# Kernel optimization log

Hardware: AMD Instinct MI355X
Metric: run time of the kernel (lower is better)

Reference implementation:

```python
import jax, jax.numpy as jnp
import numpy as np

B, S, DIM = 2, 2048, 2048
N_HEADS, N_KV_HEADS = 16, 8
HEAD_DIM = DIM // N_HEADS          # 128
KV_DIM = N_KV_HEADS * HEAD_DIM     # 1024
SKETCH = 64
ROPE_THETA = 500000.0
INV_SQRT_HD = np.float32(1.0 / np.sqrt(HEAD_DIM))


def sketch_mm(A, Sm, Bm):
    """projection_sketch_mm: approximate A @ Bm as (A S / k) @ (S^T B).
    A: (b, n, d), Sm: (b, d, k), Bm: (d, m)."""
    AS = jnp.matmul(A, Sm) / Sm.shape[-1]      # (b, n, k)
    SB = jnp.einsum('bdk,dm->bkm', Sm, Bm)     # (b, k, m)
    return jnp.matmul(AS, SB)                  # (b, n, m)


def apply_rotary(x, freqs_cis):
    """Faithful port of the module's apply_rotary_emb for one tensor.
    x: (b, s, h, hd); freqs_cis: (s, hd//2, 2) with [...,0]=cos, [...,1]=sin."""
    x2 = x.reshape(*x.shape[:-1], HEAD_DIM // 2, 2)
    f = freqs_cis[None, :, None, :, :]         # broadcast over batch & heads
    c, s = f[..., 0], f[..., 1]
    x0, x1 = x2[..., 0], x2[..., 1]
    row1 = x0 * c + x1 * s                     # dot(x, [cos, sin])
    row0 = x0 * s - x1 * c                     # dot(x, [sin, -cos]) (flip + negate)
    return jnp.stack([row0, row1], axis=-1).reshape(x.shape)


def setup_inputs() -> dict:
    key = jax.random.key(0)
    ks = jax.random.split(key, 9)
    x = jax.random.normal(ks[0], (B, S, DIM), jnp.float32)
    wq = jax.random.normal(ks[1], (DIM, DIM), jnp.float32) / np.float32(np.sqrt(DIM))
    wk = jax.random.normal(ks[2], (KV_DIM, DIM), jnp.float32) / np.float32(np.sqrt(DIM))
    wv = jax.random.normal(ks[3], (KV_DIM, DIM), jnp.float32) / np.float32(np.sqrt(DIM))
    wo = jax.random.normal(ks[4], (DIM, DIM), jnp.float32) / np.float32(np.sqrt(DIM))
    # gaussian sketch matrices (sketch_mode='gaussian'), one per batch element
    Sq = jax.random.normal(ks[5], (B, DIM, SKETCH), jnp.float32)
    Sk = jax.random.normal(ks[6], (B, DIM, SKETCH), jnp.float32)
    Sv = jax.random.normal(ks[7], (B, DIM, SKETCH), jnp.float32)
    So = jax.random.normal(ks[8], (B, DIM, SKETCH), jnp.float32)
    # RoPE table: (S, HEAD_DIM//2, 2) = stack([cos, sin])
    pos = jnp.arange(S, dtype=jnp.float32)
    inv = 1.0 / (ROPE_THETA ** (jnp.arange(0, HEAD_DIM, 2, dtype=jnp.float32) / HEAD_DIM))
    ang = pos[:, None] * inv[None, :]
    freqs_cis = jnp.stack([jnp.cos(ang), jnp.sin(ang)], axis=-1)
    return {"x": x, "wq": wq, "wk": wk, "wv": wv, "wo": wo,
            "Sq": Sq, "Sk": Sk, "Sv": Sv, "So": So, "freqs_cis": freqs_cis}


def reference(x, wq, wk, wv, wo, Sq, Sk, Sv, So, freqs_cis):
    b, s, _ = x.shape
    # RLALinear projections via projection sketch (weight stored (out, in) -> use W.T)
    xq = sketch_mm(x, Sq, wq.T).reshape(b, s, N_HEADS, HEAD_DIM)
    xk = sketch_mm(x, Sk, wk.T).reshape(b, s, N_KV_HEADS, HEAD_DIM)
    xv = sketch_mm(x, Sv, wv.T).reshape(b, s, N_KV_HEADS, HEAD_DIM)
    xq = apply_rotary(xq, freqs_cis)
    xk = apply_rotary(xk, freqs_cis)
    # repeat_kv: each kv head repeated n_rep times consecutively
    n_rep = N_HEADS // N_KV_HEADS
    k = jnp.repeat(xk, n_rep, axis=2)
    v = jnp.repeat(xv, n_rep, axis=2)
    q = xq.transpose(0, 2, 1, 3)               # (b, h, s, d)
    k = k.transpose(0, 2, 1, 3)
    v = v.transpose(0, 2, 1, 3)
    scores = jnp.einsum('bhqd,bhkd->bhqk', q, k) * INV_SQRT_HD
    mask = jnp.tril(jnp.ones((s, s), dtype=bool))
    scores = jnp.where(mask[None, None], scores, jnp.finfo(scores.dtype).min)
    probs = jax.nn.softmax(scores, axis=-1)
    out = jnp.einsum('bhqk,bhkd->bhqd', probs, v)
    out = out.transpose(0, 2, 1, 3).reshape(b, s, DIM)
    # output RLALinear via sketch
    return sketch_mm(out, So, wo.T)
```

## Files before the change

### kernel.cpp

```cpp
#include <hip/hip_runtime.h>
#include <math.h>

#define S_LEN 2048
#define DIM   2048
#define NH    16
#define NKV   8
#define HD    128
#define SKETCH 64
#define KV_DIM 1024
#define SCALE (0.08838834764831845f * 1.4426950408889634f)

typedef _Float16 half8_t  __attribute__((ext_vector_type(8)));
typedef __bf16   bf8_t    __attribute__((ext_vector_type(8)));
typedef __bf16   bf4_t    __attribute__((ext_vector_type(4)));
typedef float    f32x16_t __attribute__((ext_vector_type(16)));
typedef unsigned int uint4_t __attribute__((ext_vector_type(4)));

__global__ __launch_bounds__(256) void sbas_mfma(
    const float* __restrict__ x,
    const float* __restrict__ Sq, const float* __restrict__ Sk,
    const float* __restrict__ Sv, const float* __restrict__ So,
    const float* __restrict__ wq, const float* __restrict__ wk,
    const float* __restrict__ wv, const float* __restrict__ wo,
    float* __restrict__ SBq, float* __restrict__ SBk,
// ... 218 lines not shown
    }
    __syncthreads();
#pragma unroll
    for (int ks = 0; ks < 4; ++ks) {
      bf8_t ah = *(const bf8_t*)&Xh[w * 32 + l31][ks * 16 + h32 * 8];
      bf8_t al = *(const bf8_t*)&Xl[w * 32 + l31][ks * 16 + h32 * 8];
#pragma unroll
      for (int nt = 0; nt < 2; ++nt) {
        bf8_t bh_ = *(const bf8_t*)&Sth[nt * 32 + l31][ks * 16 + h32 * 8];
        bf8_t bl_ = *(const bf8_t*)&Stl[nt * 32 + l31][ks * 16 + h32 * 8];
        acc[nt] = __builtin_amdgcn_mfma_f32_32x32x16_bf16(ah, bh_, acc[nt], 0, 0, 0);
        acc[nt] = __builtin_amdgcn_mfma_f32_32x32x16_bf16(al, bh_, acc[nt], 0, 0, 0);
        acc[nt] = __builtin_amdgcn_mfma_f32_32x32x16_bf16(ah, bl_, acc[nt], 0, 0, 0);
      }
    }
    __syncthreads();
  }
#pragma unroll
  for (int nt = 0; nt < 2; ++nt)
#pragma unroll
    for (int r = 0; r < 16; ++r) {
      int row = row0 + w * 32 + (r & 3) + 8 * (r >> 2) + 4 * h32;
      atomicAdd(&OUT[(size_t)row * SKETCH + nt * 32 + l31],
                acc[nt][r] * (1.0f / 64.0f));
    }
}

__device__ __forceinline__ void proj_gemm_core(
    const float* __restrict__ ASb, const float* __restrict__ SBb, int Mout,
    int s0, int n0, __bf16* ASh, __bf16* ASl, __bf16* SBth, __bf16* SBtl,
    f32x16_t acc[2]) {
  const int tid = threadIdx.x, ln = tid & 63, w = tid >> 6;
  const int l31 = ln & 31, h32 = ln >> 5;
#pragma unroll
  for (int it = 0; it < 8; ++it) {
    int i = tid + it * 256;
    int r = i >> 4, c4 = (i & 15) << 2;
    float4 v = *(const float4*)(ASb + (size_t)(s0 + r) * SKETCH + c4);
    bf4_t hx, lx;
    float vv[4] = {v.x, v.y, v.z, v.w};
#pragma unroll
    for (int j = 0; j < 4; ++j) {
      __bf16 hh = (__bf16)vv[j];
      hx[j] = hh; lx[j] = (__bf16)(vv[j] - (float)hh);
    }
    *(bf4_t*)&ASh[r * 72 + c4] = hx;
    *(bf4_t*)&ASl[r * 72 + c4] = lx;
  }
#pragma unroll
  for (int it = 0; it < 4; ++it) {
    int i = tid + it * 256;
    int k = i >> 4, c4 = (i & 15) << 2;
    float4 v = *(const float4*)(SBb + (size_t)k * Mout + n0 + c4);
    float vv[4] = {v.x, v.y, v.z, v.w};
#pragma unroll
    for (int j = 0; j < 4; ++j) {
      __bf16 hh = (__bf16)vv[j];
      SBth[(c4 + j) * 72 + k] = hh;
      SBtl[(c4 + j) * 72 + k] = (__bf16)(vv[j] - (float)hh);
    }
  }
  __syncthreads();
#pragma unroll
  for (int ks = 0; ks < 4; ++ks) {
    bf8_t ah = *(const bf8_t*)&ASh[(w * 32 + l31) * 72 + ks * 16 + h32 * 8];
    bf8_t al = *(const bf8_t*)&ASl[(w * 32 + l31) * 72 + ks * 16 + h32 * 8];
#pragma unroll
    for (int nt = 0; nt < 2; ++nt) {
      bf8_t bh_ = *(const bf8_t*)&SBth[(nt * 32 + l31) * 72 + ks * 16 + h32 * 8];
      bf8_t bl_ = *(const bf8_t*)&SBtl[(nt * 32 + l31) * 72 + ks * 16 + h32 * 8];
      acc[nt] = __builtin_amdgcn_mfma_f32_32x32x16_bf16(ah, bh_, acc[nt], 0, 0, 0);
      acc[nt] = __builtin_amdgcn_mfma_f32_32x32x16_bf16(al, bh_, acc[nt], 0, 0, 0);
      acc[nt] = __builtin_amdgcn_mfma_f32_32x32x16_bf16(ah, bl_, acc[nt], 0, 0, 0);
    }
  }
}

__global__ __launch_bounds__(256) void proj_qkv(
    const float* __restrict__ ASq, const float* __restrict__ ASk,
    const float* __restrict__ ASv,
    const float* __restrict__ SBq, const float* __restrict__ SBk,
    const float* __restrict__ SBv,
    const float* __restrict__ freqs,
    _Float16* __restrict__ Qf, _Float16* __restrict__ Kf,
    _Float16* __restrict__ Vf) {
  __shared__ __bf16 ASh[128 * 72], ASl[128 * 72], SBth[64 * 72], SBtl[64 * 72];
  const int b = blockIdx.z, y = blockIdx.y;
  const float *AS, *SB;
  int Mout, nh, mt;
  _Float16* OUT;
  bool rope;
  if (y < 32)      { AS = ASq; SB = SBq; Mout = DIM;    nh = NH;  mt = y;      OUT = Qf; rope = true; }
  else if (y < 48) { AS = ASk; SB = SBk; Mout = KV_DIM; nh = NKV; mt = y - 32; OUT = Kf; rope = true; }
  else             { AS = ASv; SB = SBv; Mout = KV_DIM; nh = NKV; mt = y - 48; OUT = Vf; rope = false; }
  const int s0 = blockIdx.x * 128, n0 = mt * 64;
  f32x16_t acc[2];
#pragma unroll
  for (int nt = 0; nt < 2; ++nt)
#pragma unroll
    for (int r = 0; r < 16; ++r) acc[nt][r] = 0.0f;
  proj_gemm_core(AS + (size_t)b * S_LEN * SKETCH, SB + (size_t)b * SKETCH * Mout,
                 Mout, s0, n0, ASh, ASl, SBth, SBtl, acc);
  const int tid = threadIdx.x, ln = tid & 63, w = tid >> 6;
  const int l31 = ln & 31, h32 = ln >> 5;
  const bool meven = (l31 & 1) == 0;
#pragma unroll
  for (int nt = 0; nt < 2; ++nt) {
    const int m = n0 + nt * 32 + l31;
    const int h = m >> 7, hd = m & (HD - 1);
    const int p = hd >> 1;
#pragma unroll
    for (int r = 0; r < 16; ++r) {
      const int s = s0 + w * 32 + (r & 3) + 8 * (r >> 2) + 4 * h32;
      float v = acc[nt][r];
      float outv;
      if (rope) {
        int pi = __builtin_bit_cast(int, v);
        float part = __builtin_bit_cast(float, __builtin_amdgcn_ds_swizzle(pi, 0x041F));
        float co = freqs[((size_t)s * 64 + p) * 2 + 0];
        float si = freqs[((size_t)s * 64 + p) * 2 + 1];
        outv = meven ? (v * si - part * co) : (part * co + v * si);
      } else {
        outv = v;
      }
      OUT[(((size_t)b * nh + h) * S_LEN + s) * HD + hd] = (_Float16)outv;
    }
  }
}

__global__ __launch_bounds__(256) void proj_out(
    const float* __restrict__ ASo, const float* __restrict__ SBo,
    float* __restrict__ out) {
  __shared__ __bf16 ASh[128 * 72], ASl[128 * 72], SBth[64 * 72], SBtl[64 * 72];
  const int b = blockIdx.z;
  const int s0 = blockIdx.x * 128, n0 = blockIdx.y * 64;
  f32x16_t acc[2];
#pragma unroll
  for (int nt = 0; nt < 2; ++nt)
#pragma unroll
    for (int r = 0; r < 16; ++r) acc[nt][r] = 0.0f;
  proj_gemm_core(ASo + (size_t)b * S_LEN * SKETCH, SBo + (size_t)b * SKETCH * DIM,
                 DIM, s0, n0, ASh, ASl, SBth, SBtl, acc);
  const int tid = threadIdx.x, ln = tid & 63, w = tid >> 6;
  const int l31 = ln & 31, h32 = ln >> 5;
#pragma unroll
  for (int nt = 0; nt < 2; ++nt)
#pragma unroll
    for (int r = 0; r < 16; ++r) {
      const int s = s0 + w * 32 + (r & 3) + 8 * (r >> 2) + 4 * h32;
      out[((size_t)b * S_LEN + s) * DIM + n0 + nt * 32 + l31] = acc[nt][r];
    }
}

#define KTT 64

__global__ __launch_bounds__(256, 2) void attn_mfma(
    const _Float16* __restrict__ Qf, const _Float16* __restrict__ Kf,
    const _Float16* __restrict__ Vf, float* __restrict__ O) {
  const int bh = blockIdx.x;
  const int b = bh >> 4, h = bh & 15, g = h >> 1;
  const int qt = 31 - (int)blockIdx.y;
  const int q0 = qt * 64;

  const int tid = threadIdx.x;
  const int ln = tid & 63, w = tid >> 6;
  const int wg = w & 1, half = w >> 1;
  const int l31 = ln & 31, h32 = ln >> 5;
  const bool hb = (h32 != 0);

  __shared__ __align__(16) char smem[65536];
  char* KsH = smem + half * 16384;
  char* VtH = smem + 32768 + half * 16384;
  float* Pl = (float*)smem;
  float* Ot = (float*)smem;

  const _Float16* Kp = Kf + (size_t)(b * NKV + g) * S_LEN * HD;
  const _Float16* Vp = Vf + (size_t)(b * NKV + g) * S_LEN * HD;

  half8_t qfr[8];
  {
    const size_t qrow = (size_t)(b * NH + h) * S_LEN + q0 + wg * 32 + l31;
#pragma unroll
    for (int ks = 0; ks < 8; ++ks)
      qfr[ks] = *(const half8_t*)(Qf + qrow * HD + ks * 16 + h32 * 8);
  }

  float mrow = -1.0e30f, lrow = 0.0f;
  f32x16_t o[4];
#pragma unroll
  for (int dt = 0; dt < 4; ++dt)
#pragma unroll
    for (int r = 0; r < 16; ++r) o[dt][r] = 0.0f;

  const int wq_start = q0 + wg * 32;
  const int qq = wq_start + l31;
  const int nkt = qt + 1;
  const int nk0 = (nkt + 1) >> 1, nk1 = nkt >> 1;

  half8_t kregA[4], vregA[4], kregB[4], vregB[4];

#define LOADK(dst, t)                                                          \
  _Pragma("unroll") for (int it_ = 0; it_ < 4; ++it_) {                        \
    int i_ = tid + it_ * 256;                                                  \
    dst[it_] = *(const half8_t*)(Kp + (size_t)((t) * 64 + (i_ >> 4)) * HD +    \
                                 ((i_ & 15) << 3));                            \
  }
#define LOADV(dst, t)                                                          \
  _Pragma("unroll") for (int it_ = 0; it_ < 4; ++it_) {                        \
    int i_ = tid + it_ * 256;                                                  \
    dst[it_] = *(const half8_t*)(Vp + (size_t)((t) * 64 + (i_ & 63)) * HD +    \
                                 ((i_ >> 6) << 3));                            \
  }
#define STOREK(base, src)                                                      \
  _Pragma("unroll") for (int it_ = 0; it_ < 4; ++it_) {                        \
    int i_ = tid + it_ * 256;                                                  \
    int row_ = i_ >> 4, gg_ = (i_ & 15) ^ (row_ & 15);                         \
    *(half8_t*)((base) + row_ * 256 + (gg_ << 4)) = src[it_];                  \
  }
#define STOREV(base, src)                                                      \
  _Pragma("unroll") for (int it_ = 0; it_ < 4; ++it_) {                        \
    int i_ = tid + it_ * 256;                                                  \
    int k_ = i_ & 63, d0_ = (i_ >> 6) << 3;                                    \
    _Pragma("unroll") for (int j_ = 0; j_ < 8; ++j_) {                         \
      int d_ = d0_ + j_, gg_ = (k_ >> 3) ^ (d_ & 7);                           \
      *(_Float16*)((base) + d_ * 128 + (gg_ << 4) + ((k_ & 7) << 1)) =         \
          src[it_][j_];                                                        \
    }                                                                          \
  }

  LOADK(kregA, 0); LOADV(vregA, 0);
  if (nk1 > 0) { LOADK(kregB, nk0); LOADV(vregB, nk0); }
  STOREK(smem, kregA); STOREV(smem + 32768, vregA);
  if (nk1 > 0) { STOREK(smem + 16384, kregB); STOREV(smem + 49152, vregB); }
  __syncthreads();

  for (int i = 0; i < nk0; ++i) {
    const bool pfA = (i + 1 < nk0), pfB = (i + 1 < nk1);
    if (pfA) { LOADK(kregA, i + 1); LOADV(vregA, i + 1); }
    if (pfB) { LOADK(kregB, nk0 + i + 1); LOADV(vregB, nk0 + i + 1); }

    const int myt = half ? (nk0 + i) : i;
    const int k0 = myt * KTT;
    const bool active = (half ? (i < nk1) : true) && (k0 < wq_start + 32);

    if (active) {
      f32x16_t sc[2];
#pragma unroll
      for (int nt = 0; nt < 2; ++nt)
#pragma unroll
        for (int r = 0; r < 16; ++r) sc[nt][r] = 0.0f;
#pragma unroll
      for (int ks = 0; ks < 8; ++ks)
#pragma unroll
        for (int nt = 0; nt < 2; ++nt) {
          const int kk = nt * 32 + l31;
          half8_t kf = *(const half8_t*)(
              KsH + kk * 256 + ((((ks << 1) + h32) ^ (kk & 15)) << 4));
          sc[nt] = __builtin_amdgcn_mfma_f32_32x32x16_f16(kf, qfr[ks], sc[nt], 0, 0, 0);
        }
      const bool needMask = (k0 + KTT > wq_start);
#pragma unroll
      for (int nt = 0; nt < 2; ++nt)
#pragma unroll
        for (int r = 0; r < 16; ++r) {
          int kg = k0 + nt * 32 + (r & 3) + 8 * (r >> 2) + 4 * h32;
          float s = sc[nt][r] * SCALE;
          sc[nt][r] = (!needMask || kg <= qq) ? s : -1.0e30f;
        }
      float ml = sc[0][0];
#pragma unroll
      for (int r = 1; r < 16; ++r) ml = fmaxf(ml, sc[0][r]);
#pragma unroll
      for (int r = 0; r < 16; ++r) ml = fmaxf(ml, sc[1][r]);
      ml = fmaxf(ml, __shfl_xor(ml, 32));
      float mn = fmaxf(mrow, ml);
      float alpha = __builtin_amdgcn_exp2f(mrow - mn);
      mrow = mn;
      float ps = 0.0f;
#pragma unroll
      for (int nt = 0; nt < 2; ++nt)
#pragma unroll
        for (int r = 0; r < 16; ++r) {
          float p = __builtin_amdgcn_exp2f(sc[nt][r] - mn);
          sc[nt][r] = p;
          ps += p;
        }
      ps += __shfl_xor(ps, 32);
      lrow = lrow * alpha + ps;
#pragma unroll
      for (int dt = 0; dt < 4; ++dt)
#pragma unroll
        for (int r = 0; r < 16; ++r) o[dt][r] *= alpha;

      unsigned int pk[2][8];
#pragma unroll
      for (int nt = 0; nt < 2; ++nt)
#pragma unroll
        for (int gq = 0; gq < 8; ++gq)
          pk[nt][gq] = __builtin_bit_cast(
              unsigned int,
              __builtin_amdgcn_cvt_pkrtz(sc[nt][2 * gq], sc[nt][2 * gq + 1]));
#pragma unroll
      for (int ks2 = 0; ks2 < 4; ++ks2) {
        const int nt = ks2 >> 1, a = ks2 & 1;
        unsigned int own0 = hb ? pk[nt][4 * a + 2] : pk[nt][4 * a + 0];
        unsigned int own1 = hb ? pk[nt][4 * a + 3] : pk[nt][4 * a + 1];
        unsigned int oth0 = hb ? pk[nt][4 * a + 0] : pk[nt][4 * a + 2];
        unsigned int oth1 = hb ? pk[nt][4 * a + 1] : pk[nt][4 * a + 3];
        unsigned int rcv0 = __shfl_xor(oth0, 32);
        unsigned int rcv1 = __shfl_xor(oth1, 32);
        uint4_t fu;
        fu.x = hb ? rcv0 : own0;
        fu.y = hb ? rcv1 : own1;
        fu.z = hb ? own0 : rcv0;
        fu.w = hb ? own1 : rcv1;
        half8_t pf = __builtin_bit_cast(half8_t, fu);
#pragma unroll
        for (int dt = 0; dt < 4; ++dt) {
          const int d = dt * 32 + l31;
          half8_t vf = *(const half8_t*)(
              VtH + d * 128 + ((((ks2 << 1) + h32) ^ (d & 7)) << 4));
          o[dt] = __builtin_amdgcn_mfma_f32_32x32x16_f16(vf, pf, o[dt], 0, 0, 0);
        }
      }
    }

    if (pfA || pfB) {
      __syncthreads();
      if (pfA) { STOREK(smem, kregA); STOREV(smem + 32768, vregA); }
      if (pfB) { STOREK(smem + 16384, kregB); STOREV(smem + 49152, vregB); }
      __syncthreads();
    }
  }

  __syncthreads();
  if (w >= 2) {
    float* dst = Pl + ((size_t)(w - 2) * 64 + ln) * 68;
#pragma unroll
    for (int dt = 0; dt < 4; ++dt)
#pragma unroll
      for (int gq = 0; gq < 4; ++gq) {
        float4 vv;
        vv.x = o[dt][4 * gq + 0]; vv.y = o[dt][4 * gq + 1];
        vv.z = o[dt][4 * gq + 2]; vv.w = o[dt][4 * gq + 3];
        *(float4*)&dst[dt * 16 + gq * 4] = vv;
      }
    dst[64] = mrow; dst[65] = lrow;
  }
  __syncthreads();
  if (w < 2) {
    const float* src = Pl + ((size_t)w * 64 + ln) * 68;
    float m2 = src[64], l2 = src[65];
    float mn = fmaxf(mrow, m2);
    float a1 = __builtin_amdgcn_exp2f(mrow - mn);
    float a2 = __builtin_amdgcn_exp2f(m2 - mn);
    lrow = lrow * a1 + l2 * a2;
#pragma unroll
    for (int dt = 0; dt < 4; ++dt)
#pragma unroll
      for (int r = 0; r < 16; ++r)
        o[dt][r] = o[dt][r] * a1 + src[dt * 16 + r] * a2;
  }

  const float linv = 1.0f / lrow;
  const int s_l = tid >> 5, d_l = tid & 31;
#pragma unroll
  for (int dt = 0; dt < 4; ++dt) {
    __syncthreads();
    if (w < 2) {
#pragma unroll
      for (int gq = 0; gq < 4; ++gq) {
        float4 vv;
        vv.x = o[dt][4 * gq + 0] * linv;
        vv.y = o[dt][4 * gq + 1] * linv;
        vv.z = o[dt][4 * gq + 2] * linv;
        vv.w = o[dt][4 * gq + 3] * linv;
        *(float4*)&Ot[(wg * 32 + l31) * 36 + 8 * gq + 4 * h32] = vv;
      }
    }
    __syncthreads();
#pragma unroll
    for (int i = 0; i < 8; ++i) {
      int s = s_l + 8 * i;
      float v = Ot[s * 36 + d_l];
      O[((size_t)b * S_LEN + q0 + s) * DIM + h * HD + dt * 32 + d_l] = v;
    }
  }
#undef LOADK
#undef LOADV
#undef STOREK
#undef STOREV
}

extern "C" void kernel_launch(void* const* d_in, const int* in_sizes, int n_in,
                              void* d_out, int out_size, void* d_ws, size_t ws_size,
                              hipStream_t stream) {
  const float* x     = (const float*)d_in[0];
  const float* wq    = (const float*)d_in[1];
  const float* wk    = (const float*)d_in[2];
  const float* wv    = (const float*)d_in[3];
  const float* wo    = (const float*)d_in[4];
  const float* Sq    = (const float*)d_in[5];
  const float* Sk    = (const float*)d_in[6];
  const float* Sv    = (const float*)d_in[7];
  const float* So    = (const float*)d_in[8];
  const float* freqs = (const float*)d_in[9];
  float* out = (float*)d_out;

  const size_t AS_E = (size_t)2 * S_LEN * SKETCH;
  const size_t SBQ_E = (size_t)2 * SKETCH * DIM;
  const size_t SBK_E = (size_t)2 * SKETCH * KV_DIM;

  float* fp = (float*)d_ws;
  float* ASq = fp;  fp += AS_E;
  float* ASk = fp;  fp += AS_E;
  float* ASv = fp;  fp += AS_E;
  float* ASo = fp;  fp += AS_E;
  float* SBq = fp;  fp += SBQ_E;
  float* SBk = fp;  fp += SBK_E;
  float* SBv = fp;  fp += SBK_E;
  float* SBo = fp;  fp += SBQ_E;
  float* ATT = fp;  fp += (size_t)2 * S_LEN * DIM;
  _Float16* hp = (_Float16*)fp;
  _Float16* Qfb = hp; hp += (size_t)2 * NH  * S_LEN * HD;
  _Float16* Kfb = hp; hp += (size_t)2 * NKV * S_LEN * HD;
  _Float16* Vfb = hp; hp += (size_t)2 * NKV * S_LEN * HD;

  (void)hipMemsetAsync(ASq, 0, (4 * AS_E + 2 * SBQ_E + 2 * SBK_E) * sizeof(float), stream);

  hipLaunchKernelGGL(sbas_mfma, dim3(640), dim3(256), 0, stream,
                     x, Sq, Sk, Sv, So, wq, wk, wv, wo,
                     SBq, SBk, SBv, SBo, ASq, ASk, ASv);
  hipLaunchKernelGGL(proj_qkv, dim3(16, 64, 2), dim3(256), 0, stream,
                     ASq, ASk, ASv, SBq, SBk, SBv, freqs, Qfb, Kfb, Vfb);
  hipLaunchKernelGGL(attn_mfma, dim3(32, 32), dim3(256), 0, stream,
                     Qfb, Kfb, Vfb, ATT);
  hipLaunchKernelGGL(as_mfma, dim3(32, 8), dim3(256), 0, stream, ATT, So, ASo);
  hipLaunchKernelGGL(proj_out, dim3(16, 32, 2), dim3(256), 0, stream, ASo, SBo, out);
}
```

Before: 396.6 us.

## Shrink attention key tile to 32 with padded LDS and lazy rescaling

Cuts the attention key/value tile from 64 to 32 rows, lowering shared memory from 64KB to 35KB and raising the launch-bounds occupancy hint from 2 to 3 blocks. It also replaces the XOR-swizzled LDS layouts with padded row strides. The online softmax now rescales the output accumulator only when the running max grows by more than a threshold. The cost is twice as many loop iterations and barriers per tile, plus possible bank conflicts from the padding layout. The split of keys between the two half-blocks changes from an even split to a fixed offset of nk tiles.

```diff
diff --git a/kernel.cpp b/kernel.cpp
--- a/kernel.cpp
+++ b/kernel.cpp
@@ -394,9 +394,9 @@
     }
 }
 
-#define KTT 64
-
-__global__ __launch_bounds__(256, 2) void attn_mfma(
+#define KTT 32
+
+__global__ __launch_bounds__(256, 3) void attn_mfma(
     const _Float16* __restrict__ Qf, const _Float16* __restrict__ Kf,
     const _Float16* __restrict__ Vf, float* __restrict__ O) {
   const int bh = blockIdx.x;
@@ -410,9 +410,9 @@
   const int l31 = ln & 31, h32 = ln >> 5;
   const bool hb = (h32 != 0);
 
-  __shared__ __align__(16) char smem[65536];
-  char* KsH = smem + half * 16384;
-  char* VtH = smem + 32768 + half * 16384;
+  __shared__ __align__(16) char smem[35840];
+  char* KsH = smem + half * 8704;
+  char* VtH = smem + 17408 + half * 9216;
   float* Pl = (float*)smem;
   float* Ot = (float*)smem;
 
@@ -436,119 +436,106 @@
 
   const int wq_start = q0 + wg * 32;
   const int qq = wq_start + l31;
-  const int nkt = qt + 1;
-  const int nk0 = (nkt + 1) >> 1, nk1 = nkt >> 1;
-
-  half8_t kregA[4], vregA[4], kregB[4], vregB[4];
+  const int nk = qt + 1;
+
+  half8_t kregA[2], vregA[2], kregB[2], vregB[2];
 
 #define LOADK(dst, t)                                                          \
-  _Pragma("unroll") for (int it_ = 0; it_ < 4; ++it_) {                        \
+  _Pragma("unroll") for (int it_ = 0; it_ < 2; ++it_) {                        \
     int i_ = tid + it_ * 256;                                                  \
-    dst[it_] = *(const half8_t*)(Kp + (size_t)((t) * 64 + (i_ >> 4)) * HD +    \
+    dst[it_] = *(const half8_t*)(Kp + (size_t)((t) * 32 + (i_ >> 4)) * HD +    \
                                  ((i_ & 15) << 3));                            \
   }
 #define LOADV(dst, t)                                                          \
-  _Pragma("unroll") for (int it_ = 0; it_ < 4; ++it_) {                        \
+  _Pragma("unroll") for (int it_ = 0; it_ < 2; ++it_) {                        \
     int i_ = tid + it_ * 256;                                                  \
-    dst[it_] = *(const half8_t*)(Vp + (size_t)((t) * 64 + (i_ & 63)) * HD +    \
-                                 ((i_ >> 6) << 3));                            \
+    dst[it_] = *(const half8_t*)(Vp + (size_t)((t) * 32 + (i_ & 31)) * HD +    \
+                                 ((i_ >> 5) << 3));                            \
   }
 #define STOREK(base, src)                                                      \
-  _Pragma("unroll") for (int it_ = 0; it_ < 4; ++it_) {                        \
+  _Pragma("unroll") for (int it_ = 0; it_ < 2; ++it_) {                        \
     int i_ = tid + it_ * 256;                                                  \
-    int row_ = i_ >> 4, gg_ = (i_ & 15) ^ (row_ & 15);                         \
-    *(half8_t*)((base) + row_ * 256 + (gg_ << 4)) = src[it_];                  \
+    int row_ = i_ >> 4, gr_ = i_ & 15;                                         \
+    *(half8_t*)((base) + row_ * 272 + (gr_ << 4)) = src[it_];                  \
   }
 #define STOREV(base, src)                                                      \
-  _Pragma("unroll") for (int it_ = 0; it_ < 4; ++it_) {                        \
+  _Pragma("unroll") for (int it_ = 0; it_ < 2; ++it_) {                        \
     int i_ = tid + it_ * 256;                                                  \
-    int k_ = i_ & 63, d0_ = (i_ >> 6) << 3;                                    \
+    int k_ = i_ & 31, d0_ = (i_ >> 5) << 3;                                    \
     _Pragma("unroll") for (int j_ = 0; j_ < 8; ++j_) {                         \
-      int d_ = d0_ + j_, gg_ = (k_ >> 3) ^ (d_ & 7);                           \
-      *(_Float16*)((base) + d_ * 128 + (gg_ << 4) + ((k_ & 7) << 1)) =         \
-          src[it_][j_];                                                        \
+      *(_Float16*)((base) + (d0_ + j_) * 72 + (k_ << 1)) = src[it_][j_];       \
     }                                                                          \
   }
 
   LOADK(kregA, 0); LOADV(vregA, 0);
-  if (nk1 > 0) { LOADK(kregB, nk0); LOADV(vregB, nk0); }
-  STOREK(smem, kregA); STOREV(smem + 32768, vregA);
-  if (nk1 > 0) { STOREK(smem + 16384, kregB); STOREV(smem + 49152, vregB); }
+  LOADK(kregB, nk); LOADV(vregB, nk);
+  STOREK(smem, kregA); STOREV(smem + 17408, vregA);
+  STOREK(smem + 8704, kregB); STOREV(smem + 17408 + 9216, vregB);
   __syncthreads();
 
-  for (int i = 0; i < nk0; ++i) {
-    const bool pfA = (i + 1 < nk0), pfB = (i + 1 < nk1);
-    if (pfA) { LOADK(kregA, i + 1); LOADV(vregA, i + 1); }
-    if (pfB) { LOADK(kregB, nk0 + i + 1); LOADV(vregB, nk0 + i + 1); }
-
-    const int myt = half ? (nk0 + i) : i;
-    const int k0 = myt * KTT;
-    const bool active = (half ? (i < nk1) : true) && (k0 < wq_start + 32);
+  for (int i = 0; i < nk; ++i) {
+    const bool pf = (i + 1 < nk);
+    if (pf) {
+      LOADK(kregA, i + 1); LOADV(vregA, i + 1);
+      LOADK(kregB, nk + i + 1); LOADV(vregB, nk + i + 1);
+    }
+
+    const int t = half ? (nk + i) : i;
+    const int k0 = t * KTT;
+    const bool active = (k0 < wq_start + 32);
 
     if (active) {
-      f32x16_t sc[2];
-#pragma unroll
-      for (int nt = 0; nt < 2; ++nt)
-#pragma unroll
-        for (int r = 0; r < 16; ++r) sc[nt][r] = 0.0f;
-#pragma unroll
-      for (int ks = 0; ks < 8; ++ks)
-#pragma unroll
-        for (int nt = 0; nt < 2; ++nt) {
-          const int kk = nt * 32 + l31;
-          half8_t kf = *(const half8_t*)(
-              KsH + kk * 256 + ((((ks << 1) + h32) ^ (kk & 15)) << 4));
-          sc[nt] = __builtin_amdgcn_mfma_f32_32x32x16_f16(kf, qfr[ks], sc[nt], 0, 0, 0);
-        }
+      f32x16_t sc;
+#pragma unroll
+      for (int r = 0; r < 16; ++r) sc[r] = 0.0f;
+#pragma unroll
+      for (int ks = 0; ks < 8; ++ks) {
+        half8_t kf = *(const half8_t*)(KsH + l31 * 272 + ((ks * 16 + h32 * 8) << 1));
+        sc = __builtin_amdgcn_mfma_f32_32x32x16_f16(kf, qfr[ks], sc, 0, 0, 0);
+      }
       const bool needMask = (k0 + KTT > wq_start);
 #pragma unroll
-      for (int nt = 0; nt < 2; ++nt)
-#pragma unroll
-        for (int r = 0; r < 16; ++r) {
-          int kg = k0 + nt * 32 + (r & 3) + 8 * (r >> 2) + 4 * h32;
-          float s = sc[nt][r] * SCALE;
-          sc[nt][r] = (!needMask || kg <= qq) ? s : -1.0e30f;
-        }
-      float ml = sc[0][0];
-#pragma unroll
-      for (int r = 1; r < 16; ++r) ml = fmaxf(ml, sc[0][r]);
-#pragma unroll
-      for (int r = 0; r < 16; ++r) ml = fmaxf(ml, sc[1][r]);
+      for (int r = 0; r < 16; ++r) {
+        int kg = k0 + (r & 3) + 8 * (r >> 2) + 4 * h32;
+        float s = sc[r] * SCALE;
+        sc[r] = (!needMask || kg <= qq) ? s : -1.0e30f;
+      }
+      float ml = sc[0];
+#pragma unroll
+      for (int r = 1; r < 16; ++r) ml = fmaxf(ml, sc[r]);
       ml = fmaxf(ml, __shfl_xor(ml, 32));
-      float mn = fmaxf(mrow, ml);
-      float alpha = __builtin_amdgcn_exp2f(mrow - mn);
-      mrow = mn;
+      if (!__all(ml <= mrow + 8.0f)) {
+        float mn = fmaxf(mrow, ml);
+        float alpha = __builtin_amdgcn_exp2f(mrow - mn);
+        mrow = mn;
+        lrow *= alpha;
+#pragma unroll
+        for (int dt = 0; dt < 4; ++dt)
+#pragma unroll
+          for (int r = 0; r < 16; ++r) o[dt][r] *= alpha;
+      }
       float ps = 0.0f;
 #pragma unroll
-      for (int nt = 0; nt < 2; ++nt)
-#pragma unroll
-        for (int r = 0; r < 16; ++r) {
-          float p = __builtin_amdgcn_exp2f(sc[nt][r] - mn);
-          sc[nt][r] = p;
-          ps += p;
-        }
+      for (int r = 0; r < 16; ++r) {
+        float p = __builtin_amdgcn_exp2f(sc[r] - mrow);
+        sc[r] = p;
+        ps += p;
+      }
       ps += __shfl_xor(ps, 32);
-      lrow = lrow * alpha + ps;
-#pragma unroll
-      for (int dt = 0; dt < 4; ++dt)
-#pragma unroll
-        for (int r = 0; r < 16; ++r) o[dt][r] *= alpha;
-
-      unsigned int pk[2][8];
-#pragma unroll
-      for (int nt = 0; nt < 2; ++nt)
-#pragma unroll
-        for (int gq = 0; gq < 8; ++gq)
-          pk[nt][gq] = __builtin_bit_cast(
-              unsigned int,
-              __builtin_amdgcn_cvt_pkrtz(sc[nt][2 * gq], sc[nt][2 * gq + 1]));
-#pragma unroll
-      for (int ks2 = 0; ks2 < 4; ++ks2) {
-        const int nt = ks2 >> 1, a = ks2 & 1;
-        unsigned int own0 = hb ? pk[nt][4 * a + 2] : pk[nt][4 * a + 0];
-        unsigned int own1 = hb ? pk[nt][4 * a + 3] : pk[nt][4 * a + 1];
-        unsigned int oth0 = hb ? pk[nt][4 * a + 0] : pk[nt][4 * a + 2];
-        unsigned int oth1 = hb ? pk[nt][4 * a + 1] : pk[nt][4 * a + 3];
+      lrow += ps;
+
+      unsigned int pk[8];
+#pragma unroll
+      for (int gq = 0; gq < 8; ++gq)
+        pk[gq] = __builtin_bit_cast(
+            unsigned int,
+            __builtin_amdgcn_cvt_pkrtz(sc[2 * gq], sc[2 * gq + 1]));
+#pragma unroll
+      for (int ks2 = 0; ks2 < 2; ++ks2) {
+        unsigned int own0 = hb ? pk[4 * ks2 + 2] : pk[4 * ks2 + 0];
+        unsigned int own1 = hb ? pk[4 * ks2 + 3] : pk[4 * ks2 + 1];
+        unsigned int oth0 = hb ? pk[4 * ks2 + 0] : pk[4 * ks2 + 2];
+        unsigned int oth1 = hb ? pk[4 * ks2 + 1] : pk[4 * ks2 + 3];
         unsigned int rcv0 = __shfl_xor(oth0, 32);
         unsigned int rcv1 = __shfl_xor(oth1, 32);
         uint4_t fu;
@@ -556,21 +543,20 @@
         fu.y = hb ? rcv1 : own1;
         fu.z = hb ? own0 : rcv0;
         fu.w = hb ? own1 : rcv1;
-        half8_t pf = __builtin_bit_cast(half8_t, fu);
+        half8_t pf16 = __builtin_bit_cast(half8_t, fu);
 #pragma unroll
         for (int dt = 0; dt < 4; ++dt) {
-          const int d = dt * 32 + l31;
           half8_t vf = *(const half8_t*)(
-              VtH + d * 128 + ((((ks2 << 1) + h32) ^ (d & 7)) << 4));
-          o[dt] = __builtin_amdgcn_mfma_f32_32x32x16_f16(vf, pf, o[dt], 0, 0, 0);
-        }
-      }
-    }
-
-    if (pfA || pfB) {
+              VtH + (dt * 32 + l31) * 72 + ((ks2 * 16 + h32 * 8) << 1));
+          o[dt] = __builtin_amdgcn_mfma_f32_32x32x16_f16(vf, pf16, o[dt], 0, 0, 0);
+        }
+      }
+    }
+
+    if (pf) {
       __syncthreads();
-      if (pfA) { STOREK(smem, kregA); STOREV(smem + 32768, vregA); }
-      if (pfB) { STOREK(smem + 16384, kregB); STOREV(smem + 49152, vregB); }
+      STOREK(smem, kregA); STOREV(smem + 17408, vregA);
+      STOREK(smem + 8704, kregB); STOREV(smem + 17408 + 9216, vregB);
       __syncthreads();
     }
   }
```

After: 419.2 us. 1.06x slower.

## Load K fragments directly to registers, pad V smem, add lazy softmax rescale

Applied to the files above, without the earlier changes.

The attention kernel now loads K MFMA operand fragments straight from global memory into registers, ping-ponging between two register sets through a manually unrolled loop, so K no longer goes through shared memory. V is stored transposed in a padded layout (row stride 144 bytes) instead of an XOR swizzle, which shrinks LDS from 64KB to 36KB. The online softmax skips the rescale of the accumulators and row sum unless the new max exceeds the running max by more than 8 in log2 units. In exchange, register pressure rises (two sets of 16 half8 K fragments) and the K global loads are uncoalesced per lane. The lazy rescale lets unnormalized exponentials grow up to 2^8 before renormalizing, which risks precision loss in the fp16 probability conversion.

```diff
diff --git a/kernel.cpp b/kernel.cpp
--- a/kernel.cpp
+++ b/kernel.cpp
@@ -395,6 +395,89 @@
 }
 
 #define KTT 64
+#define VTP 144
+
+__device__ __forceinline__ void attn_step(
+    const half8_t (&kf)[2][8], const half8_t (&qfr)[8], const char* VtH,
+    int k0, int wq_start, int qq, bool hb, int h32, int l31,
+    float& mrow, float& lrow, f32x16_t (&o)[4]) {
+  f32x16_t sc[2];
+#pragma unroll
+  for (int nt = 0; nt < 2; ++nt)
+#pragma unroll
+    for (int r = 0; r < 16; ++r) sc[nt][r] = 0.0f;
+#pragma unroll
+  for (int ks = 0; ks < 8; ++ks)
+#pragma unroll
+    for (int nt = 0; nt < 2; ++nt)
+      sc[nt] = __builtin_amdgcn_mfma_f32_32x32x16_f16(kf[nt][ks], qfr[ks], sc[nt], 0, 0, 0);
+  const bool needMask = (k0 + KTT > wq_start);
+#pragma unroll
+  for (int nt = 0; nt < 2; ++nt)
+#pragma unroll
+    for (int r = 0; r < 16; ++r) {
+      int kg = k0 + nt * 32 + (r & 3) + 8 * (r >> 2) + 4 * h32;
+      float s = sc[nt][r] * SCALE;
+      sc[nt][r] = (!needMask || kg <= qq) ? s : -1.0e30f;
+    }
+  float ml = sc[0][0];
+#pragma unroll
+  for (int r = 1; r < 16; ++r) ml = fmaxf(ml, sc[0][r]);
+#pragma unroll
+  for (int r = 0; r < 16; ++r) ml = fmaxf(ml, sc[1][r]);
+  ml = fmaxf(ml, __shfl_xor(ml, 32));
+  if (!__all(ml <= mrow + 8.0f)) {
+    float mn = fmaxf(mrow, ml);
+    float alpha = __builtin_amdgcn_exp2f(mrow - mn);
+    mrow = mn;
+    lrow *= alpha;
+#pragma unroll
+    for (int dt = 0; dt < 4; ++dt)
+#pragma unroll
+      for (int r = 0; r < 16; ++r) o[dt][r] *= alpha;
+  }
+  float ps = 0.0f;
+#pragma unroll
+  for (int nt = 0; nt < 2; ++nt)
+#pragma unroll
+    for (int r = 0; r < 16; ++r) {
+      float p = __builtin_amdgcn_exp2f(sc[nt][r] - mrow);
+      sc[nt][r] = p;
+      ps += p;
+    }
+  ps += __shfl_xor(ps, 32);
+  lrow += ps;
+  unsigned int pk[2][8];
+#pragma unroll
+  for (int nt = 0; nt < 2; ++nt)
+#pragma unroll
+    for (int gq = 0; gq < 8; ++gq)
+      pk[nt][gq] = __builtin_bit_cast(
+          unsigned int,
+          __builtin_amdgcn_cvt_pkrtz(sc[nt][2 * gq], sc[nt][2 * gq + 1]));
+#pragma unroll
+  for (int ks2 = 0; ks2 < 4; ++ks2) {
+    const int nt = ks2 >> 1, a = ks2 & 1;
+    unsigned int own0 = hb ? pk[nt][4 * a + 2] : pk[nt][4 * a + 0];
+    unsigned int own1 = hb ? pk[nt][4 * a + 3] : pk[nt][4 * a + 1];
+    unsigned int oth0 = hb ? pk[nt][4 * a + 0] : pk[nt][4 * a + 2];
+    unsigned int oth1 = hb ? pk[nt][4 * a + 1] : pk[nt][4 * a + 3];
+    unsigned int rcv0 = __shfl_xor(oth0, 32);
+    unsigned int rcv1 = __shfl_xor(oth1, 32);
+    uint4_t fu;
+    fu.x = hb ? rcv0 : own0;
+    fu.y = hb ? rcv1 : own1;
+    fu.z = hb ? own0 : rcv0;
+    fu.w = hb ? own1 : rcv1;
+    half8_t pf16 = __builtin_bit_cast(half8_t, fu);
+#pragma unroll
+    for (int dt = 0; dt < 4; ++dt) {
+      half8_t vf = *(const half8_t*)(
+          VtH + (dt * 32 + l31) * VTP + ((ks2 * 16 + h32 * 8) << 1));
+      o[dt] = __builtin_amdgcn_mfma_f32_32x32x16_f16(vf, pf16, o[dt], 0, 0, 0);
+    }
+  }
+}
 
 __global__ __launch_bounds__(256, 2) void attn_mfma(
     const _Float16* __restrict__ Qf, const _Float16* __restrict__ Kf,
@@ -410,9 +493,8 @@
   const int l31 = ln & 31, h32 = ln >> 5;
   const bool hb = (h32 != 0);
 
-  __shared__ __align__(16) char smem[65536];
-  char* KsH = smem + half * 16384;
-  char* VtH = smem + 32768 + half * 16384;
+  __shared__ __align__(16) char smem[36864];
+  char* VtH = smem + half * 18432;
   float* Pl = (float*)smem;
   float* Ot = (float*)smem;
 
@@ -439,140 +521,79 @@
   const int nkt = qt + 1;
   const int nk0 = (nkt + 1) >> 1, nk1 = nkt >> 1;
 
-  half8_t kregA[4], vregA[4], kregB[4], vregB[4];
-
-#define LOADK(dst, t)                                                          \
+  half8_t ka[2][8], kb[2][8];
+  half8_t vsA[4], vsB[4];
+
+#define LOADKF(dst, ti)                                                        \
+  _Pragma("unroll") for (int nt_ = 0; nt_ < 2; ++nt_)                          \
+  _Pragma("unroll") for (int ks_ = 0; ks_ < 8; ++ks_)                          \
+    dst[nt_][ks_] = *(const half8_t*)(                                         \
+        Kp + (size_t)((ti) * 64 + nt_ * 32 + l31) * HD + ks_ * 16 + h32 * 8);
+#define LOADVS(dst, ti)                                                        \
   _Pragma("unroll") for (int it_ = 0; it_ < 4; ++it_) {                        \
     int i_ = tid + it_ * 256;                                                  \
-    dst[it_] = *(const half8_t*)(Kp + (size_t)((t) * 64 + (i_ >> 4)) * HD +    \
-                                 ((i_ & 15) << 3));                            \
-  }
-#define LOADV(dst, t)                                                          \
-  _Pragma("unroll") for (int it_ = 0; it_ < 4; ++it_) {                        \
-    int i_ = tid + it_ * 256;                                                  \
-    dst[it_] = *(const half8_t*)(Vp + (size_t)((t) * 64 + (i_ & 63)) * HD +    \
-                                 ((i_ >> 6) << 3));                            \
-  }
-#define STOREK(base, src)                                                      \
-  _Pragma("unroll") for (int it_ = 0; it_ < 4; ++it_) {                        \
-    int i_ = tid + it_ * 256;                                                  \
-    int row_ = i_ >> 4, gg_ = (i_ & 15) ^ (row_ & 15);                         \
-    *(half8_t*)((base) + row_ * 256 + (gg_ << 4)) = src[it_];                  \
-  }
-#define STOREV(base, src)                                                      \
+    dst[it_] = *(const half8_t*)(                                              \
+        Vp + (size_t)((ti) * 64 + (i_ & 63)) * HD + ((i_ >> 6) << 3));         \
+  }
+#define STOREVS(base, src)                                                     \
   _Pragma("unroll") for (int it_ = 0; it_ < 4; ++it_) {                        \
     int i_ = tid + it_ * 256;                                                  \
     int k_ = i_ & 63, d0_ = (i_ >> 6) << 3;                                    \
-    _Pragma("unroll") for (int j_ = 0; j_ < 8; ++j_) {                         \
-      int d_ = d0_ + j_, gg_ = (k_ >> 3) ^ (d_ & 7);                           \
-      *(_Float16*)((base) + d_ * 128 + (gg_ << 4) + ((k_ & 7) << 1)) =         \
-          src[it_][j_];                                                        \
-    }                                                                          \
-  }
-
-  LOADK(kregA, 0); LOADV(vregA, 0);
-  if (nk1 > 0) { LOADK(kregB, nk0); LOADV(vregB, nk0); }
-  STOREK(smem, kregA); STOREV(smem + 32768, vregA);
-  if (nk1 > 0) { STOREK(smem + 16384, kregB); STOREV(smem + 49152, vregB); }
+    _Pragma("unroll") for (int j_ = 0; j_ < 8; ++j_)                           \
+      *(_Float16*)((base) + (d0_ + j_) * VTP + (k_ << 1)) = src[it_][j_];      \
+  }
+
+  if (!half || nk1 > 0) { LOADKF(ka, half ? nk0 : 0); }
+  LOADVS(vsA, 0);
+  { const int tB = (nk1 > 0) ? nk0 : 0; LOADVS(vsB, tB); }
+  STOREVS(smem, vsA);
+  STOREVS(smem + 18432, vsB);
   __syncthreads();
 
-  for (int i = 0; i < nk0; ++i) {
-    const bool pfA = (i + 1 < nk0), pfB = (i + 1 < nk1);
-    if (pfA) { LOADK(kregA, i + 1); LOADV(vregA, i + 1); }
-    if (pfB) { LOADK(kregB, nk0 + i + 1); LOADV(vregB, nk0 + i + 1); }
-
-    const int myt = half ? (nk0 + i) : i;
-    const int k0 = myt * KTT;
-    const bool active = (half ? (i < nk1) : true) && (k0 < wq_start + 32);
-
-    if (active) {
-      f32x16_t sc[2];
-#pragma unroll
-      for (int nt = 0; nt < 2; ++nt)
-#pragma unroll
-        for (int r = 0; r < 16; ++r) sc[nt][r] = 0.0f;
-#pragma unroll
-      for (int ks = 0; ks < 8; ++ks)
-#pragma unroll
-        for (int nt = 0; nt < 2; ++nt) {
-          const int kk = nt * 32 + l31;
-          half8_t kf = *(const half8_t*)(
-              KsH + kk * 256 + ((((ks << 1) + h32) ^ (kk & 15)) << 4));
-          sc[nt] = __builtin_amdgcn_mfma_f32_32x32x16_f16(kf, qfr[ks], sc[nt], 0, 0, 0);
-        }
-      const bool needMask = (k0 + KTT > wq_start);
-#pragma unroll
-      for (int nt = 0; nt < 2; ++nt)
-#pragma unroll
-        for (int r = 0; r < 16; ++r) {
-          int kg = k0 + nt * 32 + (r & 3) + 8 * (r >> 2) + 4 * h32;
-          float s = sc[nt][r] * SCALE;
-          sc[nt][r] = (!needMask || kg <= qq) ? s : -1.0e30f;
-        }
-      float ml = sc[0][0];
-#pragma unroll
-      for (int r = 1; r < 16; ++r) ml = fmaxf(ml, sc[0][r]);
-#pragma unroll
-      for (int r = 0; r < 16; ++r) ml = fmaxf(ml, sc[1][r]);
-      ml = fmaxf(ml, __shfl_xor(ml, 32));
-      float mn = fmaxf(mrow, ml);
-      float alpha = __builtin_amdgcn_exp2f(mrow - mn);
-      mrow = mn;
-      float ps = 0.0f;
-#pragma unroll
-      for (int nt = 0; nt < 2; ++nt)
-#pragma unroll
-        for (int r = 0; r < 16; ++r) {
-          float p = __builtin_amdgcn_exp2f(sc[nt][r] - mn);
-          sc[nt][r] = p;
-          ps += p;
-        }
-      ps += __shfl_xor(ps, 32);
-      lrow = lrow * alpha + ps;
-#pragma unroll
-      for (int dt = 0; dt < 4; ++dt)
-#pragma unroll
-        for (int r = 0; r < 16; ++r) o[dt][r] *= alpha;
-
-      unsigned int pk[2][8];
-#pragma unroll
-      for (int nt = 0; nt < 2; ++nt)
-#pragma unroll
-        for (int gq = 0; gq < 8; ++gq)
-          pk[nt][gq] = __builtin_bit_cast(
-              unsigned int,
-              __builtin_amdgcn_cvt_pkrtz(sc[nt][2 * gq], sc[nt][2 * gq + 1]));
-#pragma unroll
-      for (int ks2 = 0; ks2 < 4; ++ks2) {
-        const int nt = ks2 >> 1, a = ks2 & 1;
-        unsigned int own0 = hb ? pk[nt][4 * a + 2] : pk[nt][4 * a + 0];
-        unsigned int own1 = hb ? pk[nt][4 * a + 3] : pk[nt][4 * a + 1];
-        unsigned int oth0 = hb ? pk[nt][4 * a + 0] : pk[nt][4 * a + 2];
-        unsigned int oth1 = hb ? pk[nt][4 * a + 1] : pk[nt][4 * a + 3];
-        unsigned int rcv0 = __shfl_xor(oth0, 32);
-        unsigned int rcv1 = __shfl_xor(oth1, 32);
-        uint4_t fu;
-        fu.x = hb ? rcv0 : own0;
-        fu.y = hb ? rcv1 : own1;
-        fu.z = hb ? own0 : rcv0;
-        fu.w = hb ? own1 : rcv1;
-        half8_t pf = __builtin_bit_cast(half8_t, fu);
-#pragma unroll
-        for (int dt = 0; dt < 4; ++dt) {
-          const int d = dt * 32 + l31;
-          half8_t vf = *(const half8_t*)(
-              VtH + d * 128 + ((((ks2 << 1) + h32) ^ (d & 7)) << 4));
-          o[dt] = __builtin_amdgcn_mfma_f32_32x32x16_f16(vf, pf, o[dt], 0, 0, 0);
-        }
-      }
-    }
-
-    if (pfA || pfB) {
-      __syncthreads();
-      if (pfA) { STOREK(smem, kregA); STOREV(smem + 32768, vregA); }
-      if (pfB) { STOREK(smem + 16384, kregB); STOREV(smem + 49152, vregB); }
-      __syncthreads();
-    }
+  int i = 0;
+  while (true) {
+    {
+      const bool pf = (i + 1 < nk0);
+      if (pf) {
+        if (!half || (i + 1) < nk1) { LOADKF(kb, half ? (nk0 + i + 1) : (i + 1)); }
+        LOADVS(vsA, i + 1);
+        const int tB = ((i + 1) < nk1) ? (nk0 + i + 1) : (nkt - 1);
+        LOADVS(vsB, tB);
+      }
+      const int t = half ? (nk0 + i) : i;
+      const int k0 = t * KTT;
+      const bool active = (half ? (i < nk1) : true) && (k0 < wq_start + 32);
+      if (active)
+        attn_step(ka, qfr, VtH, k0, wq_start, qq, hb, h32, l31, mrow, lrow, o);
+      if (pf) {
+        __syncthreads();
+        STOREVS(smem, vsA);
+        STOREVS(smem + 18432, vsB);
+        __syncthreads();
+      }
+    }
+    if (++i >= nk0) break;
+    {
+      const bool pf = (i + 1 < nk0);
+      if (pf) {
+        if (!half || (i + 1) < nk1) { LOADKF(ka, half ? (nk0 + i + 1) : (i + 1)); }
+        LOADVS(vsA, i + 1);
+        const int tB = ((i + 1) < nk1) ? (nk0 + i + 1) : (nkt - 1);
+        LOADVS(vsB, tB);
+      }
+      const int t = half ? (nk0 + i) : i;
+      const int k0 = t * KTT;
+      const bool active = (half ? (i < nk1) : true) && (k0 < wq_start + 32);
+      if (active)
+        attn_step(kb, qfr, VtH, k0, wq_start, qq, hb, h32, l31, mrow, lrow, o);
+      if (pf) {
+        __syncthreads();
+        STOREVS(smem, vsA);
+        STOREVS(smem + 18432, vsB);
+        __syncthreads();
+      }
+    }
+    if (++i >= nk0) break;
   }
 
   __syncthreads();
@@ -622,16 +643,15 @@
     }
     __syncthreads();
 #pragma unroll
-    for (int i = 0; i < 8; ++i) {
-      int s = s_l + 8 * i;
+    for (int ii = 0; ii < 8; ++ii) {
+      int s = s_l + 8 * ii;
       float v = Ot[s * 36 + d_l];
       O[((size_t)b * S_LEN + q0 + s) * DIM + h * HD + dt * 32 + d_l] = v;
     }
   }
-#undef LOADK
-#undef LOADV
-#undef STOREK
-#undef STOREV
+#undef LOADKF
+#undef LOADVS
+#undef STOREVS
 }
 
 extern "C" void kernel_launch(void* const* d_in, const int* in_sizes, int n_in,
```

New measurement: 451.7 us. 1.14x slower.

## Enlarge attention query tile to 128 rows with 512-thread blocks and padded LDS

Applied to the files above, without the earlier changes.

The attention kernel now handles 128 query rows per block with 8 waves instead of 64 rows with 4 waves. Four query waves share each K/V tile staged in LDS, and the causal key range is split into two contiguous halves that are merged at the end, so each K/V byte is loaded once for twice as many queries. The XOR-swizzled K and transposed-V layouts are replaced by padded row strides. Shared memory is now dynamic at 70 KB, raised once through a function attribute. The gains are less global and LDS traffic and fewer blocks. The costs are coarser causal load balance, possible bank conflicts from the padded scalar V stores, and higher LDS use per block, which may limit occupancy.

```diff
diff --git a/kernel.cpp b/kernel.cpp
--- a/kernel.cpp
+++ b/kernel.cpp
@@ -394,25 +394,29 @@
     }
 }
 
+#define QTT 128
 #define KTT 64
-
-__global__ __launch_bounds__(256, 2) void attn_mfma(
+#define KP  136
+#define VP  72
+#define ATTN_LDS 71680
+
+__global__ __launch_bounds__(512, 2) void attn_mfma(
     const _Float16* __restrict__ Qf, const _Float16* __restrict__ Kf,
     const _Float16* __restrict__ Vf, float* __restrict__ O) {
-  const int bh = blockIdx.x;
+  extern __shared__ __align__(16) char smem[];
+  const int bh = blockIdx.y;
   const int b = bh >> 4, h = bh & 15, g = h >> 1;
-  const int qt = 31 - (int)blockIdx.y;
-  const int q0 = qt * 64;
+  const int qt = 15 - (int)blockIdx.x;
+  const int q0 = qt * QTT;
 
   const int tid = threadIdx.x;
   const int ln = tid & 63, w = tid >> 6;
-  const int wg = w & 1, half = w >> 1;
+  const int wg = w & 3, half = w >> 2;
   const int l31 = ln & 31, h32 = ln >> 5;
   const bool hb = (h32 != 0);
 
-  __shared__ __align__(16) char smem[65536];
-  char* KsH = smem + half * 16384;
-  char* VtH = smem + 32768 + half * 16384;
+  char* KsH = smem + half * 17408;
+  char* VtH = smem + 34816 + half * 18432;
   float* Pl = (float*)smem;
   float* Ot = (float*)smem;
 
@@ -436,56 +440,52 @@
 
   const int wq_start = q0 + wg * 32;
   const int qq = wq_start + l31;
-  const int nkt = qt + 1;
-  const int nk0 = (nkt + 1) >> 1, nk1 = nkt >> 1;
-
-  half8_t kregA[4], vregA[4], kregB[4], vregB[4];
+  const int nk = qt + 1;
+
+  half8_t kregA[2], vregA[2], kregB[2], vregB[2];
 
 #define LOADK(dst, t)                                                          \
-  _Pragma("unroll") for (int it_ = 0; it_ < 4; ++it_) {                        \
-    int i_ = tid + it_ * 256;                                                  \
+  _Pragma("unroll") for (int it_ = 0; it_ < 2; ++it_) {                        \
+    int i_ = tid + it_ * 512;                                                  \
     dst[it_] = *(const half8_t*)(Kp + (size_t)((t) * 64 + (i_ >> 4)) * HD +    \
                                  ((i_ & 15) << 3));                            \
   }
 #define LOADV(dst, t)                                                          \
-  _Pragma("unroll") for (int it_ = 0; it_ < 4; ++it_) {                        \
-    int i_ = tid + it_ * 256;                                                  \
+  _Pragma("unroll") for (int it_ = 0; it_ < 2; ++it_) {                        \
+    int i_ = tid + it_ * 512;                                                  \
     dst[it_] = *(const half8_t*)(Vp + (size_t)((t) * 64 + (i_ & 63)) * HD +    \
                                  ((i_ >> 6) << 3));                            \
   }
 #define STOREK(base, src)                                                      \
-  _Pragma("unroll") for (int it_ = 0; it_ < 4; ++it_) {                        \
-    int i_ = tid + it_ * 256;                                                  \
-    int row_ = i_ >> 4, gg_ = (i_ & 15) ^ (row_ & 15);                         \
-    *(half8_t*)((base) + row_ * 256 + (gg_ << 4)) = src[it_];                  \
+  _Pragma("unroll") for (int it_ = 0; it_ < 2; ++it_) {                        \
+    int i_ = tid + it_ * 512;                                                  \
+    int row_ = i_ >> 4, gr_ = i_ & 15;                                         \
+    *(half8_t*)((base) + row_ * 272 + (gr_ << 4)) = src[it_];                  \
   }
 #define STOREV(base, src)                                                      \
-  _Pragma("unroll") for (int it_ = 0; it_ < 4; ++it_) {                        \
-    int i_ = tid + it_ * 256;                                                  \
+  _Pragma("unroll") for (int it_ = 0; it_ < 2; ++it_) {                        \
+    int i_ = tid + it_ * 512;                                                  \
     int k_ = i_ & 63, d0_ = (i_ >> 6) << 3;                                    \
-    _Pragma("unroll") for (int j_ = 0; j_ < 8; ++j_) {                         \
-      int d_ = d0_ + j_, gg_ = (k_ >> 3) ^ (d_ & 7);                           \
-      *(_Float16*)((base) + d_ * 128 + (gg_ << 4) + ((k_ & 7) << 1)) =         \
-          src[it_][j_];                                                        \
-    }                                                                          \
+    _Pragma("unroll") for (int j_ = 0; j_ < 8; ++j_)                           \
+      *(_Float16*)((base) + (d0_ + j_) * 144 + (k_ << 1)) = src[it_][j_];      \
   }
 
   LOADK(kregA, 0); LOADV(vregA, 0);
-  if (nk1 > 0) { LOADK(kregB, nk0); LOADV(vregB, nk0); }
-  STOREK(smem, kregA); STOREV(smem + 32768, vregA);
-  if (nk1 > 0) { STOREK(smem + 16384, kregB); STOREV(smem + 49152, vregB); }
+  LOADK(kregB, nk); LOADV(vregB, nk);
+  STOREK(smem, kregA); STOREV(smem + 34816, vregA);
+  STOREK(smem + 17408, kregB); STOREV(smem + 34816 + 18432, vregB);
   __syncthreads();
 
-  for (int i = 0; i < nk0; ++i) {
-    const bool pfA = (i + 1 < nk0), pfB = (i + 1 < nk1);
-    if (pfA) { LOADK(kregA, i + 1); LOADV(vregA, i + 1); }
-    if (pfB) { LOADK(kregB, nk0 + i + 1); LOADV(vregB, nk0 + i + 1); }
-
-    const int myt = half ? (nk0 + i) : i;
-    const int k0 = myt * KTT;
-    const bool active = (half ? (i < nk1) : true) && (k0 < wq_start + 32);
-
-    if (active) {
+  for (int i = 0; i < nk; ++i) {
+    const bool pf = (i + 1 < nk);
+    if (pf) {
+      LOADK(kregA, i + 1); LOADV(vregA, i + 1);
+      LOADK(kregB, nk + i + 1); LOADV(vregB, nk + i + 1);
+    }
+
+    const int t = half * nk + i;
+    const int k0 = t * KTT;
+    if (k0 < wq_start + 32) {
       f32x16_t sc[2];
 #pragma unroll
       for (int nt = 0; nt < 2; ++nt)
@@ -495,9 +495,8 @@
       for (int ks = 0; ks < 8; ++ks)
 #pragma unroll
         for (int nt = 0; nt < 2; ++nt) {
-          const int kk = nt * 32 + l31;
           half8_t kf = *(const half8_t*)(
-              KsH + kk * 256 + ((((ks << 1) + h32) ^ (kk & 15)) << 4));
+              KsH + (nt * 32 + l31) * 272 + ((ks * 16 + h32 * 8) << 1));
           sc[nt] = __builtin_amdgcn_mfma_f32_32x32x16_f16(kf, qfr[ks], sc[nt], 0, 0, 0);
         }
       const bool needMask = (k0 + KTT > wq_start);
@@ -556,28 +555,27 @@
         fu.y = hb ? rcv1 : own1;
         fu.z = hb ? own0 : rcv0;
         fu.w = hb ? own1 : rcv1;
-        half8_t pf = __builtin_bit_cast(half8_t, fu);
+        half8_t pf16 = __builtin_bit_cast(half8_t, fu);
 #pragma unroll
         for (int dt = 0; dt < 4; ++dt) {
-          const int d = dt * 32 + l31;
           half8_t vf = *(const half8_t*)(
-              VtH + d * 128 + ((((ks2 << 1) + h32) ^ (d & 7)) << 4));
-          o[dt] = __builtin_amdgcn_mfma_f32_32x32x16_f16(vf, pf, o[dt], 0, 0, 0);
-        }
-      }
-    }
-
-    if (pfA || pfB) {
+              VtH + (dt * 32 + l31) * 144 + ((ks2 * 16 + h32 * 8) << 1));
+          o[dt] = __builtin_amdgcn_mfma_f32_32x32x16_f16(vf, pf16, o[dt], 0, 0, 0);
+        }
+      }
+    }
+
+    if (pf) {
       __syncthreads();
-      if (pfA) { STOREK(smem, kregA); STOREV(smem + 32768, vregA); }
-      if (pfB) { STOREK(smem + 16384, kregB); STOREV(smem + 49152, vregB); }
+      STOREK(smem, kregA); STOREV(smem + 34816, vregA);
+      STOREK(smem + 17408, kregB); STOREV(smem + 34816 + 18432, vregB);
       __syncthreads();
     }
   }
 
   __syncthreads();
-  if (w >= 2) {
-    float* dst = Pl + ((size_t)(w - 2) * 64 + ln) * 68;
+  if (w >= 4) {
+    float* dst = Pl + ((size_t)(w - 4) * 64 + ln) * 68;
 #pragma unroll
     for (int dt = 0; dt < 4; ++dt)
 #pragma unroll
@@ -590,7 +588,7 @@
     dst[64] = mrow; dst[65] = lrow;
   }
   __syncthreads();
-  if (w < 2) {
+  if (w < 4) {
     const float* src = Pl + ((size_t)w * 64 + ln) * 68;
     float m2 = src[64], l2 = src[65];
     float mn = fmaxf(mrow, m2);
@@ -609,7 +607,7 @@
 #pragma unroll
   for (int dt = 0; dt < 4; ++dt) {
     __syncthreads();
-    if (w < 2) {
+    if (w < 4) {
 #pragma unroll
       for (int gq = 0; gq < 4; ++gq) {
         float4 vv;
@@ -623,7 +621,7 @@
     __syncthreads();
 #pragma unroll
     for (int i = 0; i < 8; ++i) {
-      int s = s_l + 8 * i;
+      int s = s_l + 16 * i;
       float v = Ot[s * 36 + d_l];
       O[((size_t)b * S_LEN + q0 + s) * DIM + h * HD + dt * 32 + d_l] = v;
     }
@@ -668,6 +666,14 @@
   _Float16* Kfb = hp; hp += (size_t)2 * NKV * S_LEN * HD;
   _Float16* Vfb = hp; hp += (size_t)2 * NKV * S_LEN * HD;
 
+  static bool attr_set = false;
+  if (!attr_set) {
+    (void)hipFuncSetAttribute((const void*)attn_mfma,
+                              hipFuncAttributeMaxDynamicSharedMemorySize,
+                              ATTN_LDS);
+    attr_set = true;
+  }
+
   (void)hipMemsetAsync(ASq, 0, (4 * AS_E + 2 * SBQ_E + 2 * SBK_E) * sizeof(float), stream);
 
   hipLaunchKernelGGL(sbas_mfma, dim3(640), dim3(256), 0, stream,
@@ -675,7 +681,7 @@
                      SBq, SBk, SBv, SBo, ASq, ASk, ASv);
   hipLaunchKernelGGL(proj_qkv, dim3(16, 64, 2), dim3(256), 0, stream,
                      ASq, ASk, ASv, SBq, SBk, SBv, freqs, Qfb, Kfb, Vfb);
-  hipLaunchKernelGGL(attn_mfma, dim3(32, 32), dim3(256), 0, stream,
+  hipLaunchKernelGGL(attn_mfma, dim3(16, 32), dim3(512), ATTN_LDS, stream,
                      Qfb, Kfb, Vfb, ATT);
   hipLaunchKernelGGL(as_mfma, dim3(32, 8), dim3(256), 0, stream, ATT, So, ASo);
   hipLaunchKernelGGL(proj_out, dim3(16, 32, 2), dim3(256), 0, stream, ASo, SBo, out);
```

After: 396.6 us. No clear change (+0.0%).
